# Performance work log

Measured on AMD Instinct MI355X. Metric: run time of the kernel, lower is better.

Reference implementation:

```python
import jax, jax.numpy as jnp
import numpy as np

EPS = 1e-8  # args.epsilon
B, N, D = 2, 512, 64


def _cmul(ar, ai, br, bi):
    # complex Hadamard: (ar+i ai)(br+i bi)
    return ar * br - ai * bi, ar * bi + ai * br


def _clin(Z, W, b):
    # complex linear: Z [B,2,N,din], W [2,dout,din], b [2,dout]
    yr = Z[:, 0] @ W[0].T - Z[:, 1] @ W[1].T + b[0]
    yi = Z[:, 0] @ W[1].T + Z[:, 1] @ W[0].T + b[1]
    return yr, yi


def setup_inputs() -> dict:
    key = jax.random.key(0)
    ks = jax.random.split(key, 12)
    s = 1.0 / np.sqrt(D)
    inp = {
        "Z_q": jax.random.normal(ks[0], (B, 2, N, D), jnp.float32),
        "Z_k": jax.random.normal(ks[1], (B, 2, N, D), jnp.float32),
        "Z_v": jax.random.normal(ks[2], (B, 2, N, D), jnp.float32),
        "t_measure_all": (jnp.arange(N + 1, dtype=jnp.float32) / N)[None, :],
        "Wq_w": jax.random.normal(ks[3], (2, D, D), jnp.float32) * s,
        "Wq_b": jax.random.normal(ks[4], (2, D), jnp.float32) * 0.02,
        "Wk_w": jax.random.normal(ks[5], (2, D, D), jnp.float32) * s,
        "Wk_b": jax.random.normal(ks[6], (2, D), jnp.float32) * 0.02,
        "Wv_w": jax.random.normal(ks[7], (2, D, D), jnp.float32) * s,
        "Wv_b": jax.random.normal(ks[8], (2, D), jnp.float32) * 0.02,
        "Wp_w": jax.random.normal(ks[9], (2, D, D), jnp.float32) * s,
        "Wp_b": jax.random.normal(ks[10], (2, D), jnp.float32) * 0.02,
        "lambda_imag_v": jax.random.normal(ks[11], (D // 2,), jnp.float32),
        "lambda_omega_sqrt_v": jnp.asarray(0.5, jnp.float32),
        "lambda_gamma_sqrt_v": jnp.asarray(0.5, jnp.float32),
        "noise_floor": jnp.asarray(1.0, jnp.float32),
        "tau": jnp.asarray(1.0, jnp.float32),
        "eta_param": jnp.zeros((D,), jnp.float32),
    }
    return inp


def reference(Z_q, Z_k, Z_v, t_measure_all, Wq_w, Wq_b, Wk_w, Wk_b, Wv_w, Wv_b,
              Wp_w, Wp_b, lambda_imag_v, lambda_omega_sqrt_v, lambda_gamma_sqrt_v,
              noise_floor, tau, eta_param):
    n = Z_q.shape[2]
    # eigenvalues: lambda_real_zero==1 -> real part 0; conjugate imaginary pairs
    lam_imag = jnp.concatenate([lambda_imag_v, -lambda_imag_v])  # (D,)
    lambda_h = jnp.stack([jnp.zeros_like(lam_imag), lam_imag])   # (2, D)

    t = t_measure_all[0, :-1]
    t = t / (t[-1] - t[0])

    # exp kernels exp(+/- lambda t); real part 0 => pure phase
    ph = t[:, None] * lam_imag[None, :]            # (N, D)
    ef_r, ef_i = jnp.cos(ph), jnp.sin(ph)          # exp(+lambda t) (= V_v = V_k, mat_exp)
    eb_r, eb_i = ef_r, -ef_i                       # exp(-lambda t)

    Qr, Qi = _clin(Z_q, Wq_w, Wq_b)                # (B, N, D)
    Kr, Ki = _clin(Z_k, Wk_w, Wk_b)
    Vr, Vi = _clin(Z_v, Wv_w, Wv_b)

    # backward-propagated factors U = exp(-lambda t) o {Q,K,V}
    Uq_r, Uq_i = _cmul(eb_r, eb_i, Qr, Qi)
    Uk_r, Uk_i = _cmul(eb_r, eb_i, Kr, Ki)
    Uv_r, Uv_i = _cmul(eb_r, eb_i, Vr, Vi)

    # scalar covariance kernel (zero real part -> linear-in-|dt| variance)
    lambda_omega = lambda_omega_sqrt_v ** 2
    lambda_gamma = lambda_gamma_sqrt_v ** 2 + EPS
    V_avg = lambda_omega * jnp.abs(t[:, None] - t[None, :]) + lambda_gamma  # (N, N)

    # weighted residual norm R_ij = sum_d |V_k_i o (U_q_i - U_k_j)|^2, expanded
    W2 = ef_r ** 2 + ef_i ** 2                     # (N, D)  |V_k|^2
    aq2 = Uq_r ** 2 + Uq_i ** 2
    ak2 = Uk_r ** 2 + Uk_i ** 2
    t1 = jnp.einsum('id,bid->bi', W2, aq2)[:, :, None]
    t2 = jnp.einsum('id,bjd->bij', W2, ak2)
    t3 = (jnp.einsum('bid,bjd->bij', W2[None] * Uq_r, Uk_r)
          + jnp.einsum('bid,bjd->bij', W2[None] * Uq_i, Uk_i))
    R = t1 + t2 - 2.0 * t3                         # (B, N, N)

    base = (noise_floor ** 2 + EPS) * V_avg[None] + R
    scores = -(tau ** 2) * jnp.log(base)
    mask = jnp.tril(jnp.ones((n, n), bool))
    scores = jnp.where(mask[None], scores, -jnp.inf)
    A = jax.nn.softmax(scores, axis=2)             # (B, N, N)

    # est_inner = Q_ij @ U_v (Q_ij imag part is zero)
    er = jnp.einsum('bij,bjd->bid', A, Uv_r)
    ei = jnp.einsum('bij,bjd->bid', A, Uv_i)
    estv_r, estv_i = _cmul(ef_r, ef_i, er, ei)     # V_v o est_inner

    eta = jax.nn.sigmoid(eta_param)                # (D,)
    g = jax.nn.sigmoid(eta)                        # faithful double sigmoid
    elr = (1.0 - eta) * Vr + g * estv_r
    eli = (1.0 - eta) * Vi + g * estv_i

    pr, pi = _cmul(ef_r, ef_i, elr, eli)           # mat_exp o est_latent
    P = jnp.stack([pr, pi], axis=1)
    or_, oi_ = _clin(P, Wp_w, Wp_b)
    out = jnp.stack([or_, oi_], axis=1)            # (B, 2, N, D)

    est_latent = jnp.stack([elr, eli], axis=1)
    Q_ij = jnp.stack([A, jnp.zeros_like(A)], axis=1)
    # Z_ij_hat_all[b,:,i,j,d] = V_v_i o U_v_j  (propagated estimates)
    Zr = ef_r[None, :, None, :] * Uv_r[:, None] - ef_i[None, :, None, :] * Uv_i[:, None]
    Zi = ef_r[None, :, None, :] * Uv_i[:, None] + ef_i[None, :, None, :] * Uv_r[:, None]
    Z_ij_hat_all = jnp.stack([Zr, Zi], axis=1)     # (B, 2, N, N, D)

    return est_latent, out, Q_ij, Z_ij_hat_all, lambda_h
```

## Files before the change

kernel.cpp:

```cpp
#include <hip/hip_runtime.h>
#include <math.h>

#define NB 512
#define ND 64
#define EPSF 1e-8f

typedef float v4f __attribute__((ext_vector_type(4)));

__global__ __launch_bounds__(64) void proj_kernel(
    const float* __restrict__ Zq, const float* __restrict__ Zk, const float* __restrict__ Zv,
    const float* __restrict__ tma,
    const float* __restrict__ Wq_w, const float* __restrict__ Wq_b,
    const float* __restrict__ Wk_w, const float* __restrict__ Wk_b,
    const float* __restrict__ Wv_w, const float* __restrict__ Wv_b,
    const float* __restrict__ lam_v,
    float* __restrict__ ef_r, float* __restrict__ ef_i,
    float* __restrict__ Uq_r, float* __restrict__ Uq_i,
    float* __restrict__ Uk_r, float* __restrict__ Uk_i,
    float* __restrict__ Uv_r, float* __restrict__ Uv_i,
    float* __restrict__ Vr_o, float* __restrict__ Vi_o,
    float* __restrict__ sumq, float* __restrict__ sumk,
    float* __restrict__ lam_out)
{
    const int bn = blockIdx.x;
    const int b  = bn >> 9;
    const int n  = bn & (NB - 1);
    const int d  = threadIdx.x;

    __shared__ float zqr[ND], zqi[ND], zkr[ND], zki[ND], zvr[ND], zvi[ND];
    zqr[d] = Zq[((b*2 + 0)*NB + n)*ND + d];
    zqi[d] = Zq[((b*2 + 1)*NB + n)*ND + d];
    zkr[d] = Zk[((b*2 + 0)*NB + n)*ND + d];
    zki[d] = Zk[((b*2 + 1)*NB + n)*ND + d];
    zvr[d] = Zv[((b*2 + 0)*NB + n)*ND + d];
    zvi[d] = Zv[((b*2 + 1)*NB + n)*ND + d];
    __syncthreads();

    const float lam = (d < 32) ? lam_v[d] : -lam_v[d - 32];
    const float t0    = tma[0];
    const float denom = tma[NB - 1] - t0;
    const float tn    = tma[n] / denom;
    const float ph  = tn * lam;
    const float efr = cosf(ph);
    const float efi = sinf(ph);

    if (b == 0) { ef_r[n*ND + d] = efr; ef_i[n*ND + d] = efi; }
    if (bn == 0) { lam_out[d] = 0.0f; lam_out[ND + d] = lam; }

    float qr = Wq_b[d], qi = Wq_b[ND + d];
    float kr = Wk_b[d], ki = Wk_b[ND + d];
    float vr = Wv_b[d], vi = Wv_b[ND + d];
    const int r0 = d * ND;
    const int r1 = ND*ND + d * ND;
    const float4* __restrict__ wq0 = (const float4*)&Wq_w[r0];
    const float4* __restrict__ wq1 = (const float4*)&Wq_w[r1];
    const float4* __restrict__ wk0 = (const float4*)&Wk_w[r0];
    const float4* __restrict__ wk1 = (const float4*)&Wk_w[r1];
    const float4* __restrict__ wv0 = (const float4*)&Wv_w[r0];
    const float4* __restrict__ wv1 = (const float4*)&Wv_w[r1];
    #pragma unroll
    for (int e4 = 0; e4 < ND/4; ++e4) {
        const int e = e4 * 4;
        const float4 q0 = wq0[e4], q1 = wq1[e4];
        const float4 k0 = wk0[e4], k1 = wk1[e4];
        const float4 v0 = wv0[e4], v1 = wv1[e4];
        const float zr0 = zqr[e],   zi0 = zqi[e];
        const float zr1 = zqr[e+1], zi1 = zqi[e+1];
        const float zr2 = zqr[e+2], zi2 = zqi[e+2];
        const float zr3 = zqr[e+3], zi3 = zqi[e+3];
        qr += zr0*q0.x - zi0*q1.x;  qi += zr0*q1.x + zi0*q0.x;
        qr += zr1*q0.y - zi1*q1.y;  qi += zr1*q1.y + zi1*q0.y;
        qr += zr2*q0.z - zi2*q1.z;  qi += zr2*q1.z + zi2*q0.z;
        qr += zr3*q0.w - zi3*q1.w;  qi += zr3*q1.w + zi3*q0.w;
        const float yr0 = zkr[e],   yi0 = zki[e];
        const float yr1 = zkr[e+1], yi1 = zki[e+1];
        const float yr2 = zkr[e+2], yi2 = zki[e+2];
        const float yr3 = zkr[e+3], yi3 = zki[e+3];
        kr += yr0*k0.x - yi0*k1.x;  ki += yr0*k1.x + yi0*k0.x;
        kr += yr1*k0.y - yi1*k1.y;  ki += yr1*k1.y + yi1*k0.y;
        kr += yr2*k0.z - yi2*k1.z;  ki += yr2*k1.z + yi2*k0.z;
        kr += yr3*k0.w - yi3*k1.w;  ki += yr3*k1.w + yi3*k0.w;
        const float xr0 = zvr[e],   xi0 = zvi[e];
        const float xr1 = zvr[e+1], xi1 = zvi[e+1];
        const float xr2 = zvr[e+2], xi2 = zvi[e+2];
        const float xr3 = zvr[e+3], xi3 = zvi[e+3];
        vr += xr0*v0.x - xi0*v1.x;  vi += xr0*v1.x + xi0*v0.x;
        vr += xr1*v0.y - xi1*v1.y;  vi += xr1*v1.y + xi1*v0.y;
        vr += xr2*v0.z - xi2*v1.z;  vi += xr2*v1.z + xi2*v0.z;
        vr += xr3*v0.w - xi3*v1.w;  vi += xr3*v1.w + xi3*v0.w;
    }

    const float uqr = efr*qr + efi*qi, uqi = efr*qi - efi*qr;
    const float ukr = efr*kr + efi*ki, uki = efr*ki - efi*kr;
    const float uvr = efr*vr + efi*vi, uvi = efr*vi - efi*vr;

    const int idx = bn*ND + d;
    Uq_r[idx] = uqr; Uq_i[idx] = uqi;
    Uk_r[idx] = ukr; Uk_i[idx] = uki;
    Uv_r[idx] = uvr; Uv_i[idx] = uvi;
    Vr_o[idx] = vr;  Vi_o[idx] = vi;

    float q2 = uqr*uqr + uqi*uqi;
    float k2 = ukr*ukr + uki*uki;
    #pragma unroll
    for (int off = 32; off > 0; off >>= 1) {
        q2 += __shfl_down(q2, off);
        k2 += __shfl_down(k2, off);
    }
    if (d == 0) { sumq[bn] = q2; sumk[bn] = k2; }
}

__global__ __launch_bounds__(256) void attn_fused_kernel(
    const float* __restrict__ ef_r, const float* __restrict__ ef_i,
    const float* __restrict__ Uq_r, const float* __restrict__ Uq_i,
    const float* __restrict__ Uk_r, const float* __restrict__ Uk_i,
    const float* __restrict__ Uv_r, const float* __restrict__ Uv_i,
    const float* __restrict__ Vr,  const float* __restrict__ Vi,
    const float* __restrict__ sumq, const float* __restrict__ sumk,
    const float* __restrict__ tma,
    const float* __restrict__ eta_param,
    const float* __restrict__ Wp_w, const float* __restrict__ Wp_b,
    const float* __restrict__ s_lo, const float* __restrict__ s_lg,
    const float* __restrict__ s_nf, const float* __restrict__ s_tau,
    float* __restrict__ estl_out,
    float* __restrict__ out_proj,
    float* __restrict__ Q_out,
    float* __restrict__ Z_out)
{
    const int bi   = blockIdx.x;
    const int b    = bi >> 9;
    const int i    = bi & (NB - 1);
    const int tid  = threadIdx.x;
    const int lane = tid & 63;
    const int w    = tid >> 6;
    const int sub  = lane >> 4;
    const int d4   = (lane & 15) * 4;

    __shared__ __align__(16) float sA[NB];
    __shared__ __align__(16) float qr_s[ND], qi_s[ND];
    __shared__ __align__(16) float efr_s[ND], efi_s[ND];
    __shared__ float redmax[4], redsum[4];
    __shared__ __align__(16) float erpr[4][ND], erpi[4][ND];
    __shared__ __align__(16) float pr_s[ND], pi_s[ND];

    const float t0    = tma[0];
    const float denom = tma[NB - 1] - t0;
    const float ti    = tma[i] / denom;
    const float lo    = s_lo[0] * s_lo[0];
    const float lg    = s_lg[0] * s_lg[0] + EPSF;
    const float nf2   = s_nf[0] * s_nf[0] + EPSF;
    const float tau2  = s_tau[0] * s_tau[0];
    const float t1    = sumq[bi];

    if (tid < ND) {
        qr_s[tid] = Uq_r[bi*ND + tid]; qi_s[tid] = Uq_i[bi*ND + tid];
    } else if (tid < 2*ND) {
        const int d = tid - ND;
        efr_s[d] = ef_r[i*ND + d]; efi_s[d] = ef_i[i*ND + d];
    }
    float vr_reg = 0.f, vi_reg = 0.f, eta_raw = 0.f, wb0 = 0.f, wb1 = 0.f;
    if (tid < ND) {
        vr_reg  = Vr[bi*ND + tid];
        vi_reg  = Vi[bi*ND + tid];
        eta_raw = eta_param[tid];
        wb0     = Wp_b[tid];
        wb1     = Wp_b[ND + tid];
    }
    __syncthreads();

    float lmax = -INFINITY;
    for (int j = tid; j <= i; j += 256) {
        const float4* kr4 = (const float4*)&Uk_r[(b*NB + j)*ND];
        const float4* ki4 = (const float4*)&Uk_i[(b*NB + j)*ND];
        const float4* qr4 = (const float4*)qr_s;
        const float4* qi4 = (const float4*)qi_s;
        float dot = 0.0f;
        #pragma unroll
        for (int e = 0; e < ND/4; ++e) {
            const float4 kr = kr4[e], ki = ki4[e];
            const float4 qr = qr4[e], qi = qi4[e];
            dot += qr.x*kr.x + qr.y*kr.y + qr.z*kr.z + qr.w*kr.w
                 + qi.x*ki.x + qi.y*ki.y + qi.z*ki.z + qi.w*ki.w;
        }
        const float tj   = tma[j] / denom;
        const float vavg = lo * fabsf(ti - tj) + lg;
        const float base = nf2 * vavg + t1 + sumk[b*NB + j] - 2.0f*dot;
        const float sc   = -tau2 * logf(base);
        sA[j] = sc;
        lmax = fmaxf(lmax, sc);
    }

    #pragma unroll
    for (int m = 1; m < 64; m <<= 1) lmax = fmaxf(lmax, __shfl_xor(lmax, m));
    if (lane == 0) redmax[w] = lmax;
    __syncthreads();
    const float mm = fmaxf(fmaxf(redmax[0], redmax[1]), fmaxf(redmax[2], redmax[3]));

    float lsum = 0.0f;
    for (int j = tid; j <= i; j += 256) {
        const float e = expf(sA[j] - mm);
        sA[j] = e;
        lsum += e;
    }
    #pragma unroll
    for (int m = 1; m < 64; m <<= 1) lsum += __shfl_xor(lsum, m);
    if (lane == 0) redsum[w] = lsum;
    __syncthreads();
    const float inv = 1.0f / (redsum[0] + redsum[1] + redsum[2] + redsum[3]);

    for (int j = tid; j < NB; j += 256) {
        float a = 0.0f;
        if (j <= i) a = sA[j] * inv;
        sA[j] = a;
        __builtin_nontemporal_store(a,    &Q_out[((size_t)(b*2 + 0)*NB + i)*NB + j]);
        __builtin_nontemporal_store(0.0f, &Q_out[((size_t)(b*2 + 1)*NB + i)*NB + j]);
    }
    __syncthreads();

    const float4 efr4 = *(const float4*)&efr_s[d4];
    const float4 efi4 = *(const float4*)&efi_s[d4];
    float erx = 0.f, ery = 0.f, erz = 0.f, erw = 0.f;
    float eix = 0.f, eiy = 0.f, eiz = 0.f, eiw = 0.f;
    const size_t base_r = ((size_t)(b*2 + 0)*NB + i) * (size_t)(NB*ND);
    const size_t base_i = ((size_t)(b*2 + 1)*NB + i) * (size_t)(NB*ND);
    const float* __restrict__ UvrB = &Uv_r[(size_t)(b*NB)*ND];
    const float* __restrict__ UviB = &Uv_i[(size_t)(b*NB)*ND];
    const int j0 = 4*w + sub;

    size_t roff = (size_t)j0*ND + d4;
    float4 uvr = *(const float4*)&UvrB[roff];
    float4 uvi = *(const float4*)&UviB[roff];
    float  a   = sA[j0];

    #pragma unroll 4
    for (int k = 0; k < NB/16; ++k) {
        const size_t cur = roff;
        const float4 cr = uvr, ci = uvi;
        const float  ca = a;
        if (k < NB/16 - 1) {
            roff += (size_t)16*ND;
            uvr = *(const float4*)&UvrB[roff];
            uvi = *(const float4*)&UviB[roff];
            a   = sA[j0 + 16*(k+1)];
        }
        v4f zr, zi;
        zr.x = efr4.x*cr.x - efi4.x*ci.x;  zi.x = efr4.x*ci.x + efi4.x*cr.x;
        zr.y = efr4.y*cr.y - efi4.y*ci.y;  zi.y = efr4.y*ci.y + efi4.y*cr.y;
        zr.z = efr4.z*cr.z - efi4.z*ci.z;  zi.z = efr4.z*ci.z + efi4.z*cr.z;
        zr.w = efr4.w*cr.w - efi4.w*ci.w;  zi.w = efr4.w*ci.w + efi4.w*cr.w;
        __builtin_nontemporal_store(zr, (v4f*)&Z_out[base_r + cur]);
        __builtin_nontemporal_store(zi, (v4f*)&Z_out[base_i + cur]);
        erx += ca*cr.x; ery += ca*cr.y; erz += ca*cr.z; erw += ca*cr.w;
        eix += ca*ci.x; eiy += ca*ci.y; eiz += ca*ci.z; eiw += ca*ci.w;
    }

    #pragma unroll
    for (int m = 16; m < 64; m <<= 1) {
        erx += __shfl_xor(erx, m); ery += __shfl_xor(ery, m);
        erz += __shfl_xor(erz, m); erw += __shfl_xor(erw, m);
        eix += __shfl_xor(eix, m); eiy += __shfl_xor(eiy, m);
        eiz += __shfl_xor(eiz, m); eiw += __shfl_xor(eiw, m);
    }
    if (lane < 16) {
        float4 er4; er4.x = erx; er4.y = ery; er4.z = erz; er4.w = erw;
        float4 ei4; ei4.x = eix; ei4.y = eiy; ei4.z = eiz; ei4.w = eiw;
        *(float4*)&erpr[w][lane*4] = er4;
        *(float4*)&erpi[w][lane*4] = ei4;
    }
    __syncthreads();

    if (tid < ND) {
        const int d = tid;
        const float err = erpr[0][d] + erpr[1][d] + erpr[2][d] + erpr[3][d];
        const float eii = erpi[0][d] + erpi[1][d] + erpi[2][d] + erpi[3][d];
        const float efr = efr_s[d], efi = efi_s[d];
        const float estr = efr*err - efi*eii;
        const float esti = efr*eii + efi*err;
        const float eta  = 1.0f / (1.0f + expf(-eta_raw));
        const float g    = 1.0f / (1.0f + expf(-eta));
        const float elr  = (1.0f - eta)*vr_reg + g*estr;
        const float eli  = (1.0f - eta)*vi_reg + g*esti;
        estl_out[((b*2 + 0)*NB + i)*ND + d] = elr;
        estl_out[((b*2 + 1)*NB + i)*ND + d] = eli;
        pr_s[d] = efr*elr - efi*eli;
        pi_s[d] = efr*eli + efi*elr;
    }
    __syncthreads();

    {
        float po_r = 0.0f, po_i = 0.0f;
        const float4* __restrict__ W0 = (const float4*)&Wp_w[lane*ND];
        const float4* __restrict__ W1 = (const float4*)&Wp_w[ND*ND + lane*ND];
        const int e40 = w * (ND/16);
        #pragma unroll
        for (int e4 = e40; e4 < e40 + ND/16; ++e4) {
            const float4 w0 = W0[e4], w1 = W1[e4];
            const int e = e4 * 4;
            po_r += pr_s[e]*w0.x   - pi_s[e]*w1.x;
            po_i += pr_s[e]*w1.x   + pi_s[e]*w0.x;
            po_r += pr_s[e+1]*w0.y - pi_s[e+1]*w1.y;
            po_i += pr_s[e+1]*w1.y + pi_s[e+1]*w0.y;
            po_r += pr_s[e+2]*w0.z - pi_s[e+2]*w1.z;
            po_i += pr_s[e+2]*w1.z + pi_s[e+2]*w0.z;
            po_r += pr_s[e+3]*w0.w - pi_s[e+3]*w1.w;
            po_i += pr_s[e+3]*w1.w + pi_s[e+3]*w0.w;
        }
        erpr[w][lane] = po_r; erpi[w][lane] = po_i;
    }
    __syncthreads();
    if (tid < ND) {
        const int d = tid;
        const float orr = wb0 + erpr[0][d] + erpr[1][d] + erpr[2][d] + erpr[3][d];
        const float oii = wb1 + erpi[0][d] + erpi[1][d] + erpi[2][d] + erpi[3][d];
        out_proj[((b*2 + 0)*NB + i)*ND + d] = orr;
        out_proj[((b*2 + 1)*NB + i)*ND + d] = oii;
    }
}

extern "C" void kernel_launch(void* const* d_in, const int* in_sizes, int n_in,
                              void* d_out, int out_size, void* d_ws, size_t ws_size,
                              hipStream_t stream) {
    const float* Zq   = (const float*)d_in[0];
    const float* Zk   = (const float*)d_in[1];
    const float* Zv   = (const float*)d_in[2];
    const float* tma  = (const float*)d_in[3];
    const float* Wq_w = (const float*)d_in[4];
    const float* Wq_b = (const float*)d_in[5];
    const float* Wk_w = (const float*)d_in[6];
    const float* Wk_b = (const float*)d_in[7];
    const float* Wv_w = (const float*)d_in[8];
    const float* Wv_b = (const float*)d_in[9];
    const float* Wp_w = (const float*)d_in[10];
    const float* Wp_b = (const float*)d_in[11];
    const float* lamv = (const float*)d_in[12];
    const float* s_lo = (const float*)d_in[13];
    const float* s_lg = (const float*)d_in[14];
    const float* s_nf = (const float*)d_in[15];
    const float* s_tau= (const float*)d_in[16];
    const float* etap = (const float*)d_in[17];

    float* out = (float*)d_out;
    float* o_est = out;
    float* o_out = out + 131072;
    float* o_Q   = out + 262144;
    float* o_Z   = out + 1310720;
    float* o_lam = out + 68419584;

    float* ws   = (float*)d_ws;
    float* ef_r = ws;
    float* ef_i = ws + 32768;
    float* Uq_r = ws + 65536;
    float* Uq_i = ws + 131072;
    float* Uk_r = ws + 196608;
    float* Uk_i = ws + 262144;
    float* Uv_r = ws + 327680;
    float* Uv_i = ws + 393216;
    float* Vr   = ws + 458752;
    float* Vi   = ws + 524288;
    float* sumq = ws + 589824;
    float* sumk = ws + 590848;

    proj_kernel<<<2*NB, 64, 0, stream>>>(Zq, Zk, Zv, tma, Wq_w, Wq_b, Wk_w, Wk_b,
        Wv_w, Wv_b, lamv, ef_r, ef_i, Uq_r, Uq_i, Uk_r, Uk_i, Uv_r, Uv_i,
        Vr, Vi, sumq, sumk, o_lam);

    attn_fused_kernel<<<2*NB, 256, 0, stream>>>(ef_r, ef_i, Uq_r, Uq_i, Uk_r, Uk_i,
        Uv_r, Uv_i, Vr, Vi, sumq, sumk, tma, etap, Wp_w, Wp_b,
        s_lo, s_lg, s_nf, s_tau, o_est, o_out, o_Q, o_Z);
}
```

Before: 338.6 us.

## Split Z_hat write into separate streaming kernel from attention

Moves the large Z_ij_hat output generation out of the fused attention kernel into a dedicated zhat_kernel with twice as many blocks, each covering half the j-rows. The attention kernel now only reads Uv for the A·Uv reduction without software prefetch, and its Q stores become regular stores instead of nontemporal ones. The intent is to let the bandwidth-bound Z_hat write run as a simple, highly parallel streaming kernel rather than being serialized behind the softmax work. The cost is rereading Uv in a second pass and paying one more kernel launch.

```diff
diff --git a/kernel.cpp b/kernel.cpp
--- a/kernel.cpp
+++ b/kernel.cpp
@@ -110,7 +110,7 @@
     if (d == 0) { sumq[bn] = q2; sumk[bn] = k2; }
 }
 
-__global__ __launch_bounds__(256) void attn_fused_kernel(
+__global__ __launch_bounds__(256) void attn_kernel(
     const float* __restrict__ ef_r, const float* __restrict__ ef_i,
     const float* __restrict__ Uq_r, const float* __restrict__ Uq_i,
     const float* __restrict__ Uk_r, const float* __restrict__ Uk_i,
@@ -124,8 +124,7 @@
     const float* __restrict__ s_nf, const float* __restrict__ s_tau,
     float* __restrict__ estl_out,
     float* __restrict__ out_proj,
-    float* __restrict__ Q_out,
-    float* __restrict__ Z_out)
+    float* __restrict__ Q_out)
 {
     const int bi   = blockIdx.x;
     const int b    = bi >> 9;
@@ -212,8 +211,8 @@
         float a = 0.0f;
         if (j <= i) a = sA[j] * inv;
         sA[j] = a;
-        __builtin_nontemporal_store(a,    &Q_out[((size_t)(b*2 + 0)*NB + i)*NB + j]);
-        __builtin_nontemporal_store(0.0f, &Q_out[((size_t)(b*2 + 1)*NB + i)*NB + j]);
+        Q_out[((size_t)(b*2 + 0)*NB + i)*NB + j] = a;
+        Q_out[((size_t)(b*2 + 1)*NB + i)*NB + j] = 0.0f;
     }
     __syncthreads();
 
@@ -221,37 +220,19 @@
     const float4 efi4 = *(const float4*)&efi_s[d4];
     float erx = 0.f, ery = 0.f, erz = 0.f, erw = 0.f;
     float eix = 0.f, eiy = 0.f, eiz = 0.f, eiw = 0.f;
-    const size_t base_r = ((size_t)(b*2 + 0)*NB + i) * (size_t)(NB*ND);
-    const size_t base_i = ((size_t)(b*2 + 1)*NB + i) * (size_t)(NB*ND);
     const float* __restrict__ UvrB = &Uv_r[(size_t)(b*NB)*ND];
     const float* __restrict__ UviB = &Uv_i[(size_t)(b*NB)*ND];
     const int j0 = 4*w + sub;
 
-    size_t roff = (size_t)j0*ND + d4;
-    float4 uvr = *(const float4*)&UvrB[roff];
-    float4 uvi = *(const float4*)&UviB[roff];
-    float  a   = sA[j0];
-
     #pragma unroll 4
     for (int k = 0; k < NB/16; ++k) {
-        const size_t cur = roff;
-        const float4 cr = uvr, ci = uvi;
-        const float  ca = a;
-        if (k < NB/16 - 1) {
-            roff += (size_t)16*ND;
-            uvr = *(const float4*)&UvrB[roff];
-            uvi = *(const float4*)&UviB[roff];
-            a   = sA[j0 + 16*(k+1)];
-        }
-        v4f zr, zi;
-        zr.x = efr4.x*cr.x - efi4.x*ci.x;  zi.x = efr4.x*ci.x + efi4.x*cr.x;
-        zr.y = efr4.y*cr.y - efi4.y*ci.y;  zi.y = efr4.y*ci.y + efi4.y*cr.y;
-        zr.z = efr4.z*cr.z - efi4.z*ci.z;  zi.z = efr4.z*ci.z + efi4.z*cr.z;
-        zr.w = efr4.w*cr.w - efi4.w*ci.w;  zi.w = efr4.w*ci.w + efi4.w*cr.w;
-        __builtin_nontemporal_store(zr, (v4f*)&Z_out[base_r + cur]);
-        __builtin_nontemporal_store(zi, (v4f*)&Z_out[base_i + cur]);
-        erx += ca*cr.x; ery += ca*cr.y; erz += ca*cr.z; erw += ca*cr.w;
-        eix += ca*ci.x; eiy += ca*ci.y; eiz += ca*ci.z; eiw += ca*ci.w;
+        const int j = 16*k + j0;
+        const size_t roff = (size_t)j*ND + d4;
+        const float4 uvr = *(const float4*)&UvrB[roff];
+        const float4 uvi = *(const float4*)&UviB[roff];
+        const float a = sA[j];
+        erx += a*uvr.x; ery += a*uvr.y; erz += a*uvr.z; erw += a*uvr.w;
+        eix += a*uvi.x; eiy += a*uvi.y; eiz += a*uvi.z; eiw += a*uvi.w;
     }
 
     #pragma unroll
@@ -314,6 +295,45 @@
         const float oii = wb1 + erpi[0][d] + erpi[1][d] + erpi[2][d] + erpi[3][d];
         out_proj[((b*2 + 0)*NB + i)*ND + d] = orr;
         out_proj[((b*2 + 1)*NB + i)*ND + d] = oii;
+    }
+}
+
+__global__ __launch_bounds__(256) void zhat_kernel(
+    const float* __restrict__ ef_r, const float* __restrict__ ef_i,
+    const float* __restrict__ Uv_r, const float* __restrict__ Uv_i,
+    float* __restrict__ Z_out)
+{
+    const int blk  = blockIdx.x;
+    const int bi   = blk >> 1;
+    const int half = blk & 1;
+    const int b    = bi >> 9;
+    const int i    = bi & (NB - 1);
+    const int tid  = threadIdx.x;
+
+    const int d4    = (tid & 15) * 4;
+    const int jrow0 = (tid >> 4) + half * 256;
+
+    const float4 er4 = *(const float4*)&ef_r[i*ND + d4];
+    const float4 ei4 = *(const float4*)&ef_i[i*ND + d4];
+
+    const size_t base_r = ((size_t)(b*2 + 0)*NB + i) * (size_t)(NB*ND);
+    const size_t base_i = ((size_t)(b*2 + 1)*NB + i) * (size_t)(NB*ND);
+    const float* __restrict__ UvrB = &Uv_r[(size_t)(b*NB)*ND];
+    const float* __restrict__ UviB = &Uv_i[(size_t)(b*NB)*ND];
+
+    #pragma unroll
+    for (int k = 0; k < 16; ++k) {
+        const int j = jrow0 + 16*k;
+        const size_t off = (size_t)j*ND + d4;
+        const float4 uvr = *(const float4*)&UvrB[off];
+        const float4 uvi = *(const float4*)&UviB[off];
+        v4f zr, zi;
+        zr.x = er4.x*uvr.x - ei4.x*uvi.x;  zi.x = er4.x*uvi.x + ei4.x*uvr.x;
+        zr.y = er4.y*uvr.y - ei4.y*uvi.y;  zi.y = er4.y*uvi.y + ei4.y*uvr.y;
+        zr.z = er4.z*uvr.z - ei4.z*uvi.z;  zi.z = er4.z*uvi.z + ei4.z*uvr.z;
+        zr.w = er4.w*uvr.w - ei4.w*uvi.w;  zi.w = er4.w*uvi.w + ei4.w*uvr.w;
+        __builtin_nontemporal_store(zr, (v4f*)&Z_out[base_r + off]);
+        __builtin_nontemporal_store(zi, (v4f*)&Z_out[base_i + off]);
     }
 }
 
@@ -364,7 +384,9 @@
         Wv_w, Wv_b, lamv, ef_r, ef_i, Uq_r, Uq_i, Uk_r, Uk_i, Uv_r, Uv_i,
         Vr, Vi, sumq, sumk, o_lam);
 
-    attn_fused_kernel<<<2*NB, 256, 0, stream>>>(ef_r, ef_i, Uq_r, Uq_i, Uk_r, Uk_i,
+    attn_kernel<<<2*NB, 256, 0, stream>>>(ef_r, ef_i, Uq_r, Uq_i, Uk_r, Uk_i,
         Uv_r, Uv_i, Vr, Vi, sumq, sumk, tma, etap, Wp_w, Wp_b,
-        s_lo, s_lg, s_nf, s_tau, o_est, o_out, o_Q, o_Z);
+        s_lo, s_lg, s_nf, s_tau, o_est, o_out, o_Q);
+
+    zhat_kernel<<<4*NB, 256, 0, stream>>>(ef_r, ef_i, Uv_r, Uv_i, o_Z);
 }
```

New measurement: 375.6 us. +10.9%, slower.
